# Performance work log

Measured on AMD Instinct MI355X. Metric: run time of the kernel, lower is better.

## Reference

```python
import jax, jax.numpy as jnp
import numpy as np

C_S = 128
C_T = 128
C_OUT = 128


def _proj(x, W, b):
    # 1x1x1 Conv3d == per-voxel linear over channel dim. x: [B, Cin, T, H, W]
    return jnp.einsum('oc,bcthw->bothw', W, x) + b[None, :, None, None, None]


def setup_inputs() -> dict:
    key = jax.random.key(0)
    ks = jax.random.split(key, 12)
    B, T, H, W = 4, 4, 32, 32
    spatial_features = jax.random.normal(ks[0], (B, T, C_S, H, W), dtype=jnp.float32)
    temporal_features = jax.random.normal(ks[1], (B, C_T, T, H, W), dtype=jnp.float32)
    def w(k, o, i):
        return jax.random.normal(k, (o, i), dtype=jnp.float32) * (i ** -0.5)
    return {
        'spatial_features': spatial_features,
        'temporal_features': temporal_features,
        'Wq': w(ks[2], C_OUT, C_S), 'bq': jnp.zeros((C_OUT,), jnp.float32),
        'Wk': w(ks[3], C_OUT, C_T), 'bk': jnp.zeros((C_OUT,), jnp.float32),
        'Wv': w(ks[4], C_OUT, C_T), 'bv': jnp.zeros((C_OUT,), jnp.float32),
        'Wo': w(ks[5], C_OUT, C_OUT), 'bo': jnp.zeros((C_OUT,), jnp.float32),
    }


def reference(spatial_features, temporal_features, Wq, bq, Wk, bk, Wv, bv, Wo, bo):
    B, T, C_s, H, W = spatial_features.shape
    N = T * H * W
    scale = C_OUT ** -0.5
    # permute(0,2,1,3,4): [B, T, C_s, H, W] -> [B, C_s, T, H, W]
    x_s = jnp.transpose(spatial_features, (0, 2, 1, 3, 4))
    q = _proj(x_s, Wq, bq)                 # [B, C_out, T, H, W]
    k = _proj(temporal_features, Wk, bk)   # [B, C_out, T, H, W]
    v = _proj(temporal_features, Wv, bv)   # [B, C_out, T, H, W]
    Q = q.reshape(B, C_OUT, N).transpose(0, 2, 1)  # [B, N, C]
    K = k.reshape(B, C_OUT, N)                     # [B, C, N]
    V = v.reshape(B, C_OUT, N).transpose(0, 2, 1)  # [B, N, C]
    attn = jax.nn.softmax(jnp.einsum('bnc,bcm->bnm', Q, K) * scale, axis=2)  # [B, N, N]
    out = jnp.einsum('bnm,bmc->bnc', attn, V)      # [B, N, C]
    out = out.transpose(0, 2, 1).reshape(B, C_OUT, T, H, W)
    return _proj(out, Wo, bo)
```

## Files before the change

kernel.cpp:

```cpp
#include <hip/hip_runtime.h>
#include <cstddef>

#define NDIM 4096
#define SCALE_L2E 0.12751741843533886f
#define BIAS_L2E  11.541560327111707f

typedef _Float16 h8 __attribute__((ext_vector_type(8)));
typedef _Float16 h4 __attribute__((ext_vector_type(4)));
typedef _Float16 h2 __attribute__((ext_vector_type(2)));
typedef float    f4 __attribute__((ext_vector_type(4)));

__device__ __forceinline__ void gld_lds16(const void* g, void* l) {
    __builtin_amdgcn_global_load_lds(
        (const __attribute__((address_space(1))) void*)g,
        (__attribute__((address_space(3))) void*)l, 16, 0, 0);
}

__device__ __forceinline__ h8 cvt_w_frag(const float* wp) {
    const float4 u0 = *(const float4*)wp;
    const float4 u1 = *(const float4*)(wp + 4);
    h8 f;
    f[0]=(_Float16)u0.x; f[1]=(_Float16)u0.y; f[2]=(_Float16)u0.z; f[3]=(_Float16)u0.w;
    f[4]=(_Float16)u1.x; f[5]=(_Float16)u1.y; f[6]=(_Float16)u1.z; f[7]=(_Float16)u1.w;
    return f;
}

__global__ __launch_bounds__(256) void prep_w_kernel(
    const float* __restrict__ Wq, const float* __restrict__ Wk,
    const float* __restrict__ Wv, const float* __restrict__ Wo,
    _Float16* __restrict__ Whf)
{
    const int gid = blockIdx.x * 256 + threadIdx.x;
    const int mat = gid >> 11, rem = gid & 2047;
    const int ot = rem >> 8, ks = (rem >> 6) & 3, l = rem & 63;
    const float* src = mat == 0 ? Wq : mat == 1 ? Wk : mat == 2 ? Wv : Wo;
    const h8 f = cvt_w_frag(src + (size_t)(16 * ot + (l & 15)) * 128 + 32 * ks + 8 * (l >> 4));
    *(h8*)(Whf + (size_t)gid * 8) = f;
}

__global__ __launch_bounds__(256, 3) void proj_qkv_kernel(
    const float* __restrict__ spatial, const float* __restrict__ temporal,
    const _Float16* __restrict__ Whf,
    const float* __restrict__ bq, const float* __restrict__ bk,
    const float* __restrict__ bv,
    _Float16* __restrict__ Qh, _Float16* __restrict__ Kh, _Float16* __restrict__ Vt)
{
    __shared__ __align__(16) _Float16 Xl[32 * 136];
    const int tid = threadIdx.x;
    const int n0  = blockIdx.x * 32;
    const int b   = blockIdx.y;
    const int p   = blockIdx.z;
    const float* __restrict__ bias = (p == 0) ? bq : (p == 1) ? bk : bv;

    {
        const float* src; size_t rs;
        if (p == 0) { const int t = n0 >> 10, hw0 = n0 & 1023;
            src = spatial + (((size_t)(b * 4 + t) * 128) << 10) + hw0; rs = 1024; }
        else { src = temporal + ((size_t)(b * 128) << 12) + n0; rs = 4096; }
        #pragma unroll
        for (int i = 0; i < 2; ++i) {
            const int ii = tid + 256 * i;
            const int c2 = ii >> 3, j = ii & 7;
            const float4 v0 = *(const float4*)(src + (size_t)(2 * c2) * rs + 4 * j);
            const float4 v1 = *(const float4*)(src + (size_t)(2 * c2 + 1) * rs + 4 * j);
            const float a0[4] = {v0.x, v0.y, v0.z, v0.w};
            const float a1[4] = {v1.x, v1.y, v1.z, v1.w};
            #pragma unroll
            for (int u = 0; u < 4; ++u) {
                h2 pk; pk[0] = (_Float16)a0[u]; pk[1] = (_Float16)a1[u];
                *(h2*)&Xl[(4 * j + u) * 136 + 2 * c2] = pk;
            }
        }
    }
    __syncthreads();

    const int w = tid >> 6, lane = tid & 63, n16 = tid & 15, q4 = (tid >> 4) & 3;

    h8 wf[2][4];
    #pragma unroll
    for (int otl = 0; otl < 2; ++otl)
        #pragma unroll
        for (int ks = 0; ks < 4; ++ks)
            wf[otl][ks] = *(const h8*)(Whf + ((size_t)(((p * 8 + 2 * w + otl) * 4 + ks)) << 9)
                                           + lane * 8);
    h8 xf[2][4];
    #pragma unroll
    for (int ns = 0; ns < 2; ++ns)
        #pragma unroll
        for (int ks = 0; ks < 4; ++ks)
            xf[ns][ks] = *(const h8*)&Xl[(16 * ns + n16) * 136 + 32 * ks + 8 * q4];

    if (p < 2) {
        f4 acc[2][2];
        #pragma unroll
        for (int i = 0; i < 2; ++i) { acc[i][0] = (f4)0.0f; acc[i][1] = (f4)0.0f; }
        #pragma unroll
        for (int otl = 0; otl < 2; ++otl)
            #pragma unroll
            for (int ns = 0; ns < 2; ++ns)
                #pragma unroll
                for (int ks = 0; ks < 4; ++ks)
                    acc[otl][ns] = __builtin_amdgcn_mfma_f32_16x16x32_f16(
                        wf[otl][ks], xf[ns][ks], acc[otl][ns], 0, 0, 0);
        _Float16* __restrict__ dst = (p == 0) ? Qh : Kh;
        #pragma unroll
        for (int otl = 0; otl < 2; ++otl) {
            const float4 bb = *(const float4*)&bias[16 * (2 * w + otl) + 4 * q4];
            #pragma unroll
            for (int ns = 0; ns < 2; ++ns) {
                h4 r;
                r[0]=(_Float16)(acc[otl][ns][0]+bb.x); r[1]=(_Float16)(acc[otl][ns][1]+bb.y);
                r[2]=(_Float16)(acc[otl][ns][2]+bb.z); r[3]=(_Float16)(acc[otl][ns][3]+bb.w);
                *(h4*)(dst + ((size_t)b * NDIM + n0 + 16 * ns + n16) * 128
                           + 16 * (2 * w + otl) + 4 * q4) = r;
            }
        }
    } else {
        f4 acc[2][2];
        #pragma unroll
        for (int i = 0; i < 2; ++i) { acc[i][0] = (f4)0.0f; acc[i][1] = (f4)0.0f; }
        #pragma unroll
        for (int ns = 0; ns < 2; ++ns)
            #pragma unroll
            for (int otl = 0; otl < 2; ++otl)
                #pragma unroll
                for (int ks = 0; ks < 4; ++ks)
                    acc[ns][otl] = __builtin_amdgcn_mfma_f32_16x16x32_f16(
                        xf[ns][ks], wf[otl][ks], acc[ns][otl], 0, 0, 0);
        #pragma unroll
        for (int ns = 0; ns < 2; ++ns)
            #pragma unroll
            for (int otl = 0; otl < 2; ++otl) {
                const float bb = bias[16 * (2 * w + otl) + n16];
                h4 r;
                r[0]=(_Float16)(acc[ns][otl][0]+bb); r[1]=(_Float16)(acc[ns][otl][1]+bb);
                r[2]=(_Float16)(acc[ns][otl][2]+bb); r[3]=(_Float16)(acc[ns][otl][3]+bb);
                *(h4*)(Vt + ((size_t)(b * 128 + 16 * (2 * w + otl) + n16) << 12)
                          + n0 + 16 * ns + 4 * q4) = r;
            }
    }
}

__global__ __launch_bounds__(256, 2) void attn_kernel(
    const _Float16* __restrict__ Qh, const _Float16* __restrict__ Kh,
    const _Float16* __restrict__ Vt, _Float16* __restrict__ Opart,
    float* __restrict__ lpart)
{
    __shared__ __align__(16) _Float16 sh[30720];

    const int tid  = threadIdx.x;
    const int w    = tid >> 6, lane = tid & 63;
    const int g    = w >> 1,  p    = w & 1;
    const int n16  = lane & 15, q4 = lane >> 4;

    const int id = blockIdx.x + 32 * blockIdx.y + 128 * blockIdx.z;
    const int pi = (id & 7) + 8 * (id >> 8);
    const int qt = (id >> 3) & 31;
    const int hf = pi & 3, b = pi >> 2;
    const int n0 = qt * 128;
    const int mb = hf * 1024;

    const int r4 = lane >> 4, c16 = lane & 15;
    const _Float16* kg0 = Kh + ((size_t)b * NDIM + mb + 8 * w + r4) * 128
                             + ((c16 * 8) ^ ((r4 & 7) << 3));
    const _Float16* kg1 = Kh + ((size_t)b * NDIM + mb + 8 * w + 4 + r4) * 128
                             + ((c16 * 8) ^ (((4 + r4) & 7) << 3));
    const int vr = lane >> 2, vc4 = lane & 3;
    const _Float16* vg0 = Vt + (((size_t)(b * 128 + 32 * w + vr)) << 12) + mb + vc4 * 8;
    const _Float16* vg1 = vg0 + ((size_t)16 << 12);

    const int kd = (8 * w) * 128;
    const int vd = (32 * w) * 32;

    gld_lds16(kg0, sh + kd);            gld_lds16(kg1, sh + kd + 512);
    gld_lds16(vg0, sh + 8192 + vd);     gld_lds16(vg1, sh + 8192 + vd + 512);
    kg0 += 32 * 128; kg1 += 32 * 128; vg0 += 32; vg1 += 32;

    h8 qf[4][4];
    {
        const _Float16* Qb = Qh + ((size_t)b * NDIM + n0 + 64 * g + n16) * 128;
        #pragma unroll
        for (int qs = 0; qs < 4; ++qs)
            #pragma unroll
            for (int ks = 0; ks < 4; ++ks)
                qf[qs][ks] = *(const h8*)(Qb + (size_t)(16 * qs) * 128 + 32 * ks + 8 * q4);
    }

    f4 oacc[4][4];
    #pragma unroll
    for (int i = 0; i < 4; ++i)
        #pragma unroll
        for (int j = 0; j < 4; ++j) oacc[i][j] = (f4)0.0f;
    float lsum[4] = {0.0f, 0.0f, 0.0f, 0.0f};

    const int kx = (n16 & 7) << 3;
    const int krow = (16 * p + n16) * 128;

    for (int it = 0; it < 32; ++it) {
        __syncthreads();
        const int cur = it & 1;
        _Float16* __restrict__ Pg = sh + 20480 + cur * 5120 + g * 2560;
        const _Float16* __restrict__ Pp = sh + 20480 + (cur ^ 1) * 5120 + g * 2560;

        if (it < 31) {
            _Float16* kdst = sh + (cur ^ 1) * 4096 + kd;
            gld_lds16(kg0, kdst); gld_lds16(kg1, kdst + 512);
            const int vst = (it + 1) % 3;
            _Float16* vdst = sh + 8192 + vst * 4096 + vd;
            gld_lds16(vg0, vdst); gld_lds16(vg1, vdst + 512);
            kg0 += 32 * 128; kg1 += 32 * 128; vg0 += 32; vg1 += 32;
        }

        if (it > 0) {
            const int vrd = (it - 1) % 3;
            const _Float16* __restrict__ VP = sh + 8192 + vrd * 4096;
            h8 pf[4], vf[4];
            #pragma unroll
            for (int qs = 0; qs < 4; ++qs)
                pf[qs] = *(const h8*)&Pp[(16 * qs + n16) * 40 + 8 * q4];
            #pragma unroll
            for (int ct = 0; ct < 4; ++ct)
                vf[ct] = *(const h8*)&VP[(64 * p + 16 * ct + n16) * 32 + 8 * q4];
            __builtin_amdgcn_s_setprio(1);
            #pragma unroll
            for (int qs = 0; qs < 4; ++qs)
                #pragma unroll
                for (int ct = 0; ct < 4; ++ct)
                    oacc[qs][ct] = __builtin_amdgcn_mfma_f32_16x16x32_f16(
                        pf[qs], vf[ct], oacc[qs][ct], 0, 0, 0);
            __builtin_amdgcn_s_setprio(0);
        }

        f4 sacc[4];
        #pragma unroll
        for (int qs = 0; qs < 4; ++qs) sacc[qs] = (f4)0.0f;
        {
            const _Float16* __restrict__ KB = sh + cur * 4096;
            h8 kf[4];
            #pragma unroll
            for (int ks = 0; ks < 4; ++ks)
                kf[ks] = *(const h8*)&KB[krow + ((32 * ks + 8 * q4) ^ kx)];
            __builtin_amdgcn_s_setprio(1);
            #pragma unroll
            for (int ks = 0; ks < 4; ++ks)
                #pragma unroll
                for (int qs = 0; qs < 4; ++qs)
                    sacc[qs] = __builtin_amdgcn_mfma_f32_16x16x32_f16(
                        kf[ks], qf[qs][ks], sacc[qs], 0, 0, 0);
            __builtin_amdgcn_s_setprio(0);
        }

        #pragma unroll
        for (int qs = 0; qs < 4; ++qs) {
            h4 pk;
            #pragma unroll
            for (int r = 0; r < 4; ++r) {
                const float e = __builtin_amdgcn_exp2f(fmaf(sacc[qs][r], SCALE_L2E, -BIAS_L2E));
                lsum[qs] += e;
                pk[r] = (_Float16)e;
            }
            *(h4*)&Pg[(16 * qs + n16) * 40 + 16 * p + 4 * q4] = pk;
        }
    }

    __syncthreads();
    {
        const _Float16* __restrict__ Pp = sh + 20480 + 5120 + g * 2560;
        const _Float16* __restrict__ VP = sh + 8192 + 1 * 4096;
        h8 pf[4], vf[4];
        #pragma unroll
        for (int qs = 0; qs < 4; ++qs)
            pf[qs] = *(const h8*)&Pp[(16 * qs + n16) * 40 + 8 * q4];
        #pragma unroll
        for (int ct = 0; ct < 4; ++ct)
            vf[ct] = *(const h8*)&VP[(64 * p + 16 * ct + n16) * 32 + 8 * q4];
        #pragma unroll
        for (int qs = 0; qs < 4; ++qs)
            #pragma unroll
            for (int ct = 0; ct < 4; ++ct)
                oacc[qs][ct] = __builtin_amdgcn_mfma_f32_16x16x32_f16(
                    pf[qs], vf[ct], oacc[qs][ct], 0, 0, 0);
    }

    #pragma unroll
    for (int qs = 0; qs < 4; ++qs) {
        lsum[qs] += __shfl_xor(lsum[qs], 16, 64);
        lsum[qs] += __shfl_xor(lsum[qs], 32, 64);
    }
    if (q4 == 0) {
        float* lb = lpart + ((size_t)((hf * 2 + p) * 4 + b)) * NDIM + n0 + 64 * g;
        #pragma unroll
        for (int qs = 0; qs < 4; ++qs) lb[16 * qs + n16] = lsum[qs];
    }

    __syncthreads();
    #pragma unroll
    for (int qs = 0; qs < 4; ++qs)
        #pragma unroll
        for (int ct = 0; ct < 4; ++ct)
            #pragma unroll
            for (int r = 0; r < 4; ++r)
                sh[(64 * g + 16 * qs + 4 * q4 + r) * 136 + 64 * p + 16 * ct + n16] =
                    (_Float16)oacc[qs][ct][r];
    __syncthreads();
    const size_t ob = ((size_t)(hf * 4 + b) * NDIM + n0) * 128;
    #pragma unroll
    for (int i = 0; i < 8; ++i) {
        const int ii  = tid + 256 * i;
        const int row = ii >> 4, c8 = (ii & 15) * 8;
        *(int4*)(Opart + ob + (size_t)row * 128 + c8) = *(const int4*)&sh[row * 136 + c8];
    }
}

__global__ __launch_bounds__(256, 2) void proj_final_kernel(
    const _Float16* __restrict__ Opart, const float* __restrict__ lpart,
    const _Float16* __restrict__ Whf, const float* __restrict__ bo,
    float* __restrict__ out)
{
    __shared__ __align__(16) _Float16 Xl[32 * 136];
    __shared__ float lrow[32];
    __shared__ __align__(16) float Ofin[128 * 36];
    const int tid = threadIdx.x;
    const int n0  = blockIdx.x * 32;
    const int b   = blockIdx.y;

    if (tid < 32) {
        float l = 0.0f;
        #pragma unroll
        for (int h8i = 0; h8i < 8; ++h8i)
            l += lpart[((size_t)(h8i * 4 + b)) * NDIM + n0 + tid];
        lrow[tid] = 1.0f / l;
    }
    float vals[2][8];
    int rows[2], c8s[2];
    #pragma unroll
    for (int i = 0; i < 2; ++i) {
        const int ii = tid + 256 * i;
        rows[i] = ii >> 4; c8s[i] = (ii & 15) * 8;
        #pragma unroll
        for (int j = 0; j < 8; ++j) vals[i][j] = 0.0f;
        #pragma unroll
        for (int hf = 0; hf < 4; ++hf) {
            const h8 o = *(const h8*)(Opart + ((size_t)(hf * 4 + b) * NDIM + n0 + rows[i]) * 128
                                      + c8s[i]);
            #pragma unroll
            for (int j = 0; j < 8; ++j) vals[i][j] += (float)o[j];
        }
    }
    __syncthreads();
    #pragma unroll
    for (int i = 0; i < 2; ++i) {
        const float linv = lrow[rows[i]];
        h8 r;
        #pragma unroll
        for (int j = 0; j < 8; ++j) r[j] = (_Float16)(vals[i][j] * linv);
        *(h8*)&Xl[rows[i] * 136 + c8s[i]] = r;
    }
    __syncthreads();

    const int w = tid >> 6, lane = tid & 63, n16 = tid & 15, q4 = (tid >> 4) & 3;

    h8 wf[2][4];
    #pragma unroll
    for (int otl = 0; otl < 2; ++otl)
        #pragma unroll
        for (int ks = 0; ks < 4; ++ks)
            wf[otl][ks] = *(const h8*)(Whf + ((size_t)(((3 * 8 + 2 * w + otl) * 4 + ks)) << 9)
                                           + lane * 8);
    h8 xf[2][4];
    #pragma unroll
    for (int ns = 0; ns < 2; ++ns)
        #pragma unroll
        for (int ks = 0; ks < 4; ++ks)
            xf[ns][ks] = *(const h8*)&Xl[(16 * ns + n16) * 136 + 32 * ks + 8 * q4];

    f4 acc[2][2];
    #pragma unroll
    for (int i = 0; i < 2; ++i) { acc[i][0] = (f4)0.0f; acc[i][1] = (f4)0.0f; }
    #pragma unroll
    for (int otl = 0; otl < 2; ++otl)
        #pragma unroll
        for (int ns = 0; ns < 2; ++ns)
            #pragma unroll
            for (int ks = 0; ks < 4; ++ks)
                acc[otl][ns] = __builtin_amdgcn_mfma_f32_16x16x32_f16(
                    wf[otl][ks], xf[ns][ks], acc[otl][ns], 0, 0, 0);

    #pragma unroll
    for (int otl = 0; otl < 2; ++otl) {
        const float4 bb = *(const float4*)&bo[16 * (2 * w + otl) + 4 * q4];
        const float bias[4] = {bb.x, bb.y, bb.z, bb.w};
        #pragma unroll
        for (int ns = 0; ns < 2; ++ns)
            #pragma unroll
            for (int r = 0; r < 4; ++r)
                Ofin[(16 * (2 * w + otl) + 4 * q4 + r) * 36 + 16 * ns + n16] =
                    acc[otl][ns][r] + bias[r];
    }
    __syncthreads();
    #pragma unroll
    for (int i = 0; i < 4; ++i) {
        const int ii  = tid + 256 * i;
        const int row = ii >> 3, j = ii & 7;
        *(float4*)(out + (((size_t)(b * 128 + row)) << 12) + n0 + 4 * j) =
            *(const float4*)&Ofin[row * 36 + 4 * j];
    }
}

extern "C" void kernel_launch(void* const* d_in, const int* in_sizes, int n_in,
                              void* d_out, int out_size, void* d_ws, size_t ws_size,
                              hipStream_t stream)
{
    const float* spatial  = (const float*)d_in[0];
    const float* temporal = (const float*)d_in[1];
    const float* Wq = (const float*)d_in[2];
    const float* bq = (const float*)d_in[3];
    const float* Wk = (const float*)d_in[4];
    const float* bk = (const float*)d_in[5];
    const float* Wv = (const float*)d_in[6];
    const float* bv = (const float*)d_in[7];
    const float* Wo = (const float*)d_in[8];
    const float* bo = (const float*)d_in[9];

    char* ws = (char*)d_ws;
    _Float16* Qh    = (_Float16*)(ws);
    _Float16* Kh    = (_Float16*)(ws + (4u  << 20));
    _Float16* Vt    = (_Float16*)(ws + (8u  << 20));
    _Float16* Opart = (_Float16*)(ws + (12u << 20));
    float*    lpart = (float*)   (ws + (28u << 20));
    _Float16* Whf   = (_Float16*)(ws + (28u << 20) + (512u << 10));

    prep_w_kernel<<<32, 256, 0, stream>>>(Wq, Wk, Wv, Wo, Whf);
    proj_qkv_kernel<<<dim3(128, 4, 3), 256, 0, stream>>>(
        spatial, temporal, Whf, bq, bk, bv, Qh, Kh, Vt);
    attn_kernel<<<dim3(32, 4, 4), 256, 0, stream>>>(Qh, Kh, Vt, Opart, lpart);
    proj_final_kernel<<<dim3(128, 4), 256, 0, stream>>>(Opart, lpart, Whf, bo,
                                                        (float*)d_out);
}
```

Measured before the change: 136.4 us.

## Switch attention to 32x32x16 MFMA with register-resident P and per-wave query rows

Rewrites the attention inner loop to use 32x32x16 MFMA tiles, where each wave owns 32 query rows and the full key tile. The exponentiated scores stay in registers as the A operand of the PV MFMA, so the LDS staging buffer for P and its extra synchronisation are removed. The change also swaps the V triple buffer for a double buffer with XOR swizzling and halves the lpart partial sums per row. It cuts LDS traffic and shared memory size, but adds more accumulator registers, which may pressure occupancy.

```diff
diff --git a/kernel.cpp b/kernel.cpp
--- a/kernel.cpp
+++ b/kernel.cpp
@@ -9,6 +9,7 @@
 typedef _Float16 h4 __attribute__((ext_vector_type(4)));
 typedef _Float16 h2 __attribute__((ext_vector_type(2)));
 typedef float    f4 __attribute__((ext_vector_type(4)));
+typedef float    f32x16 __attribute__((ext_vector_type(16)));
 
 __device__ __forceinline__ void gld_lds16(const void* g, void* l) {
     __builtin_amdgcn_global_load_lds(
@@ -146,12 +147,12 @@
     const _Float16* __restrict__ Vt, _Float16* __restrict__ Opart,
     float* __restrict__ lpart)
 {
-    __shared__ __align__(16) _Float16 sh[30720];
+    __shared__ __align__(16) _Float16 sh[17408];
 
     const int tid  = threadIdx.x;
     const int w    = tid >> 6, lane = tid & 63;
-    const int g    = w >> 1,  p    = w & 1;
-    const int n16  = lane & 15, q4 = lane >> 4;
+    const int g    = w;
+    const int lq   = lane & 31, kh = lane >> 5;
 
     const int id = blockIdx.x + 32 * blockIdx.y + 128 * blockIdx.z;
     const int pi = (id & 7) + 8 * (id >> 8);
@@ -162,13 +163,13 @@
 
     const int r4 = lane >> 4, c16 = lane & 15;
     const _Float16* kg0 = Kh + ((size_t)b * NDIM + mb + 8 * w + r4) * 128
-                             + ((c16 * 8) ^ ((r4 & 7) << 3));
+                             + ((c16 * 8) ^ (r4 << 3));
     const _Float16* kg1 = Kh + ((size_t)b * NDIM + mb + 8 * w + 4 + r4) * 128
-                             + ((c16 * 8) ^ (((4 + r4) & 7) << 3));
+                             + ((c16 * 8) ^ ((4 + r4) << 3));
     const int vr = lane >> 2, vc4 = lane & 3;
-    const _Float16* vg0 = Vt + (((size_t)(b * 128 + 32 * w + vr)) << 12) + mb + vc4 * 8;
+    const _Float16* vg0 = Vt + (((size_t)(b * 128 + 32 * w + vr)) << 12) + mb
+                             + 8 * (vc4 ^ ((vr >> 1) & 3));
     const _Float16* vg1 = vg0 + ((size_t)16 << 12);
-
     const int kd = (8 * w) * 128;
     const int vd = (32 * w) * 32;
 
@@ -176,132 +177,117 @@
     gld_lds16(vg0, sh + 8192 + vd);     gld_lds16(vg1, sh + 8192 + vd + 512);
     kg0 += 32 * 128; kg1 += 32 * 128; vg0 += 32; vg1 += 32;
 
-    h8 qf[4][4];
+    h8 qf[8];
     {
-        const _Float16* Qb = Qh + ((size_t)b * NDIM + n0 + 64 * g + n16) * 128;
-        #pragma unroll
-        for (int qs = 0; qs < 4; ++qs)
-            #pragma unroll
-            for (int ks = 0; ks < 4; ++ks)
-                qf[qs][ks] = *(const h8*)(Qb + (size_t)(16 * qs) * 128 + 32 * ks + 8 * q4);
-    }
-
-    f4 oacc[4][4];
-    #pragma unroll
-    for (int i = 0; i < 4; ++i)
-        #pragma unroll
-        for (int j = 0; j < 4; ++j) oacc[i][j] = (f4)0.0f;
-    float lsum[4] = {0.0f, 0.0f, 0.0f, 0.0f};
-
-    const int kx = (n16 & 7) << 3;
-    const int krow = (16 * p + n16) * 128;
+        const _Float16* Qb = Qh + ((size_t)b * NDIM + n0 + 32 * g + lq) * 128 + 8 * kh;
+        #pragma unroll
+        for (int ks = 0; ks < 8; ++ks)
+            qf[ks] = *(const h8*)(Qb + 16 * ks);
+    }
+
+    f32x16 oacc[4];
+    #pragma unroll
+    for (int i = 0; i < 4; ++i) oacc[i] = (f32x16)0.0f;
+    float la0 = 0.0f, la1 = 0.0f;
+    h8 pf0, pf1, vfr[4][2];
+
+    const int krow = lq * 128;
+    const int kxr  = lq & 7;
 
     for (int it = 0; it < 32; ++it) {
         __syncthreads();
         const int cur = it & 1;
-        _Float16* __restrict__ Pg = sh + 20480 + cur * 5120 + g * 2560;
-        const _Float16* __restrict__ Pp = sh + 20480 + (cur ^ 1) * 5120 + g * 2560;
 
         if (it < 31) {
             _Float16* kdst = sh + (cur ^ 1) * 4096 + kd;
+            _Float16* vdst = sh + 8192 + (cur ^ 1) * 4096 + vd;
             gld_lds16(kg0, kdst); gld_lds16(kg1, kdst + 512);
-            const int vst = (it + 1) % 3;
-            _Float16* vdst = sh + 8192 + vst * 4096 + vd;
             gld_lds16(vg0, vdst); gld_lds16(vg1, vdst + 512);
             kg0 += 32 * 128; kg1 += 32 * 128; vg0 += 32; vg1 += 32;
         }
 
-        if (it > 0) {
-            const int vrd = (it - 1) % 3;
-            const _Float16* __restrict__ VP = sh + 8192 + vrd * 4096;
-            h8 pf[4], vf[4];
-            #pragma unroll
-            for (int qs = 0; qs < 4; ++qs)
-                pf[qs] = *(const h8*)&Pp[(16 * qs + n16) * 40 + 8 * q4];
-            #pragma unroll
-            for (int ct = 0; ct < 4; ++ct)
-                vf[ct] = *(const h8*)&VP[(64 * p + 16 * ct + n16) * 32 + 8 * q4];
-            __builtin_amdgcn_s_setprio(1);
-            #pragma unroll
-            for (int qs = 0; qs < 4; ++qs)
-                #pragma unroll
-                for (int ct = 0; ct < 4; ++ct)
-                    oacc[qs][ct] = __builtin_amdgcn_mfma_f32_16x16x32_f16(
-                        pf[qs], vf[ct], oacc[qs][ct], 0, 0, 0);
-            __builtin_amdgcn_s_setprio(0);
-        }
-
-        f4 sacc[4];
-        #pragma unroll
-        for (int qs = 0; qs < 4; ++qs) sacc[qs] = (f4)0.0f;
+        f32x16 sa = (f32x16)0.0f, sb = (f32x16)0.0f;
         {
             const _Float16* __restrict__ KB = sh + cur * 4096;
-            h8 kf[4];
-            #pragma unroll
-            for (int ks = 0; ks < 4; ++ks)
-                kf[ks] = *(const h8*)&KB[krow + ((32 * ks + 8 * q4) ^ kx)];
+            #pragma unroll
+            for (int ks = 0; ks < 4; ++ks) {
+                const h8 kf = *(const h8*)&KB[krow + 8 * ((2 * ks + kh) ^ kxr)];
+                sa = __builtin_amdgcn_mfma_f32_32x32x16_f16(kf, qf[ks], sa, 0, 0, 0);
+            }
+            #pragma unroll
+            for (int ks = 4; ks < 8; ++ks) {
+                const h8 kf = *(const h8*)&KB[krow + 8 * ((2 * ks + kh) ^ kxr)];
+                sb = __builtin_amdgcn_mfma_f32_32x32x16_f16(kf, qf[ks], sb, 0, 0, 0);
+            }
+        }
+
+        if (it > 0) {
             __builtin_amdgcn_s_setprio(1);
             #pragma unroll
-            for (int ks = 0; ks < 4; ++ks)
+            for (int cb = 0; cb < 4; ++cb) {
+                oacc[cb] = __builtin_amdgcn_mfma_f32_32x32x16_f16(pf0, vfr[cb][0], oacc[cb], 0, 0, 0);
+                oacc[cb] = __builtin_amdgcn_mfma_f32_32x32x16_f16(pf1, vfr[cb][1], oacc[cb], 0, 0, 0);
+            }
+            __builtin_amdgcn_s_setprio(0);
+        }
+
+        {
+            const _Float16* __restrict__ VB = sh + 8192 + cur * 4096;
+            #pragma unroll
+            for (int cb = 0; cb < 4; ++cb) {
+                const int cbase = (32 * cb + lq) * 32;
+                const int sx = lq & 6;
                 #pragma unroll
-                for (int qs = 0; qs < 4; ++qs)
-                    sacc[qs] = __builtin_amdgcn_mfma_f32_16x16x32_f16(
-                        kf[ks], qf[qs][ks], sacc[qs], 0, 0, 0);
-            __builtin_amdgcn_s_setprio(0);
-        }
-
-        #pragma unroll
-        for (int qs = 0; qs < 4; ++qs) {
-            h4 pk;
-            #pragma unroll
-            for (int r = 0; r < 4; ++r) {
-                const float e = __builtin_amdgcn_exp2f(fmaf(sacc[qs][r], SCALE_L2E, -BIAS_L2E));
-                lsum[qs] += e;
-                pk[r] = (_Float16)e;
-            }
-            *(h4*)&Pg[(16 * qs + n16) * 40 + 16 * p + 4 * q4] = pk;
-        }
-    }
-
-    __syncthreads();
+                for (int kk = 0; kk < 2; ++kk) {
+                    const h4 lo = *(const h4*)&VB[cbase + 4 * ((4 * kk + kh) ^ sx)];
+                    const h4 hi = *(const h4*)&VB[cbase + 4 * ((4 * kk + 2 + kh) ^ sx)];
+                    h8 v;
+                    v[0]=lo[0]; v[1]=lo[1]; v[2]=lo[2]; v[3]=lo[3];
+                    v[4]=hi[0]; v[5]=hi[1]; v[6]=hi[2]; v[7]=hi[3];
+                    vfr[cb][kk] = v;
+                }
+            }
+        }
+
+        #pragma unroll
+        for (int r = 0; r < 8; ++r) {
+            const float e = __builtin_amdgcn_exp2f(
+                fmaf(sa[r], SCALE_L2E, fmaf(sb[r], SCALE_L2E, -BIAS_L2E)));
+            if (r & 1) la1 += e; else la0 += e;
+            pf0[r] = (_Float16)e;
+        }
+        #pragma unroll
+        for (int r = 8; r < 16; ++r) {
+            const float e = __builtin_amdgcn_exp2f(
+                fmaf(sa[r], SCALE_L2E, fmaf(sb[r], SCALE_L2E, -BIAS_L2E)));
+            if (r & 1) la1 += e; else la0 += e;
+            pf1[r - 8] = (_Float16)e;
+        }
+    }
+
     {
-        const _Float16* __restrict__ Pp = sh + 20480 + 5120 + g * 2560;
-        const _Float16* __restrict__ VP = sh + 8192 + 1 * 4096;
-        h8 pf[4], vf[4];
-        #pragma unroll
-        for (int qs = 0; qs < 4; ++qs)
-            pf[qs] = *(const h8*)&Pp[(16 * qs + n16) * 40 + 8 * q4];
-        #pragma unroll
-        for (int ct = 0; ct < 4; ++ct)
-            vf[ct] = *(const h8*)&VP[(64 * p + 16 * ct + n16) * 32 + 8 * q4];
-        #pragma unroll
-        for (int qs = 0; qs < 4; ++qs)
-            #pragma unroll
-            for (int ct = 0; ct < 4; ++ct)
-                oacc[qs][ct] = __builtin_amdgcn_mfma_f32_16x16x32_f16(
-                    pf[qs], vf[ct], oacc[qs][ct], 0, 0, 0);
-    }
-
-    #pragma unroll
-    for (int qs = 0; qs < 4; ++qs) {
-        lsum[qs] += __shfl_xor(lsum[qs], 16, 64);
-        lsum[qs] += __shfl_xor(lsum[qs], 32, 64);
-    }
-    if (q4 == 0) {
-        float* lb = lpart + ((size_t)((hf * 2 + p) * 4 + b)) * NDIM + n0 + 64 * g;
-        #pragma unroll
-        for (int qs = 0; qs < 4; ++qs) lb[16 * qs + n16] = lsum[qs];
-    }
-
-    __syncthreads();
-    #pragma unroll
-    for (int qs = 0; qs < 4; ++qs)
-        #pragma unroll
-        for (int ct = 0; ct < 4; ++ct)
-            #pragma unroll
-            for (int r = 0; r < 4; ++r)
-                sh[(64 * g + 16 * qs + 4 * q4 + r) * 136 + 64 * p + 16 * ct + n16] =
-                    (_Float16)oacc[qs][ct][r];
+        __builtin_amdgcn_s_setprio(1);
+        #pragma unroll
+        for (int cb = 0; cb < 4; ++cb) {
+            oacc[cb] = __builtin_amdgcn_mfma_f32_32x32x16_f16(pf0, vfr[cb][0], oacc[cb], 0, 0, 0);
+            oacc[cb] = __builtin_amdgcn_mfma_f32_32x32x16_f16(pf1, vfr[cb][1], oacc[cb], 0, 0, 0);
+        }
+        __builtin_amdgcn_s_setprio(0);
+    }
+
+    float lsum = la0 + la1;
+    lsum += __shfl_xor(lsum, 32, 64);
+    if (lane < 32)
+        lpart[((size_t)(hf * 4 + b)) * NDIM + n0 + 32 * g + lq] = lsum;
+
+    __syncthreads();
+    #pragma unroll
+    for (int cb = 0; cb < 4; ++cb)
+        #pragma unroll
+        for (int r = 0; r < 16; ++r) {
+            const int qrow = 32 * g + (r & 3) + 8 * (r >> 2) + 4 * kh;
+            sh[qrow * 136 + 32 * cb + lq] = (_Float16)oacc[cb][r];
+        }
     __syncthreads();
     const size_t ob = ((size_t)(hf * 4 + b) * NDIM + n0) * 128;
     #pragma unroll
@@ -327,8 +313,8 @@
     if (tid < 32) {
         float l = 0.0f;
         #pragma unroll
-        for (int h8i = 0; h8i < 8; ++h8i)
-            l += lpart[((size_t)(h8i * 4 + b)) * NDIM + n0 + tid];
+        for (int h4i = 0; h4i < 4; ++h4i)
+            l += lpart[((size_t)(h4i * 4 + b)) * NDIM + n0 + tid];
         lrow[tid] = 1.0f / l;
     }
     float vals[2][8];
```

New measurement: 144.5 us. 1.06x slower.

## Double attention block to 512 threads with 32-row query slices per wave group

Applied to the files above, without the earlier changes.

The attention kernel now runs 8 waves per block instead of 4. Each wave group handles 32 query rows rather than 64, which halves the per-thread Q fragments and accumulators and so lowers register pressure. Each thread issues one K and one V global-to-LDS load per tile instead of two. The V tile in LDS gets an XOR swizzle to cut bank conflicts. More waves share each K/V tile, which should improve latency hiding, at the cost of more synchronisation participants per barrier.

```diff
diff --git a/kernel.cpp b/kernel.cpp
--- a/kernel.cpp
+++ b/kernel.cpp
@@ -141,7 +141,7 @@
     }
 }
 
-__global__ __launch_bounds__(256, 2) void attn_kernel(
+__global__ __launch_bounds__(512, 4) void attn_kernel(
     const _Float16* __restrict__ Qh, const _Float16* __restrict__ Kh,
     const _Float16* __restrict__ Vt, _Float16* __restrict__ Opart,
     float* __restrict__ lpart)
@@ -160,70 +160,64 @@
     const int n0 = qt * 128;
     const int mb = hf * 1024;
 
-    const int r4 = lane >> 4, c16 = lane & 15;
-    const _Float16* kg0 = Kh + ((size_t)b * NDIM + mb + 8 * w + r4) * 128
-                             + ((c16 * 8) ^ ((r4 & 7) << 3));
-    const _Float16* kg1 = Kh + ((size_t)b * NDIM + mb + 8 * w + 4 + r4) * 128
-                             + ((c16 * 8) ^ (((4 + r4) & 7) << 3));
-    const int vr = lane >> 2, vc4 = lane & 3;
-    const _Float16* vg0 = Vt + (((size_t)(b * 128 + 32 * w + vr)) << 12) + mb + vc4 * 8;
-    const _Float16* vg1 = vg0 + ((size_t)16 << 12);
-
-    const int kd = (8 * w) * 128;
-    const int vd = (32 * w) * 32;
-
-    gld_lds16(kg0, sh + kd);            gld_lds16(kg1, sh + kd + 512);
-    gld_lds16(vg0, sh + 8192 + vd);     gld_lds16(vg1, sh + 8192 + vd + 512);
-    kg0 += 32 * 128; kg1 += 32 * 128; vg0 += 32; vg1 += 32;
-
-    h8 qf[4][4];
+    const int kr = tid >> 4, kc = tid & 15;
+    const _Float16* kg = Kh + ((size_t)b * NDIM + mb + kr) * 128
+                            + 8 * (kc ^ (kr & 7));
+    const int vr = tid >> 2, vc = tid & 3;
+    const _Float16* vg = Vt + (((size_t)(b * 128 + vr)) << 12) + mb
+                            + 8 * (vc ^ ((vr >> 1) & 3));
+    const int ld = tid * 8;
+
+    gld_lds16(kg, sh + ld);
+    gld_lds16(vg, sh + 8192 + ld);
+    kg += 32 * 128; vg += 32;
+
+    h8 qf[2][4];
     {
-        const _Float16* Qb = Qh + ((size_t)b * NDIM + n0 + 64 * g + n16) * 128;
-        #pragma unroll
-        for (int qs = 0; qs < 4; ++qs)
+        const _Float16* Qb = Qh + ((size_t)b * NDIM + n0 + 32 * g + n16) * 128;
+        #pragma unroll
+        for (int qs = 0; qs < 2; ++qs)
             #pragma unroll
             for (int ks = 0; ks < 4; ++ks)
                 qf[qs][ks] = *(const h8*)(Qb + (size_t)(16 * qs) * 128 + 32 * ks + 8 * q4);
     }
 
-    f4 oacc[4][4];
-    #pragma unroll
-    for (int i = 0; i < 4; ++i)
+    f4 oacc[2][4];
+    #pragma unroll
+    for (int i = 0; i < 2; ++i)
         #pragma unroll
         for (int j = 0; j < 4; ++j) oacc[i][j] = (f4)0.0f;
-    float lsum[4] = {0.0f, 0.0f, 0.0f, 0.0f};
-
-    const int kx = (n16 & 7) << 3;
+    float lsum[2] = {0.0f, 0.0f};
+
+    const int kx   = (n16 & 7) << 3;
     const int krow = (16 * p + n16) * 128;
 
     for (int it = 0; it < 32; ++it) {
         __syncthreads();
         const int cur = it & 1;
-        _Float16* __restrict__ Pg = sh + 20480 + cur * 5120 + g * 2560;
-        const _Float16* __restrict__ Pp = sh + 20480 + (cur ^ 1) * 5120 + g * 2560;
+        _Float16* __restrict__ Pb = sh + 20480 + cur * 5120;
+        const _Float16* __restrict__ Pp = sh + 20480 + (cur ^ 1) * 5120;
 
         if (it < 31) {
-            _Float16* kdst = sh + (cur ^ 1) * 4096 + kd;
-            gld_lds16(kg0, kdst); gld_lds16(kg1, kdst + 512);
-            const int vst = (it + 1) % 3;
-            _Float16* vdst = sh + 8192 + vst * 4096 + vd;
-            gld_lds16(vg0, vdst); gld_lds16(vg1, vdst + 512);
-            kg0 += 32 * 128; kg1 += 32 * 128; vg0 += 32; vg1 += 32;
+            gld_lds16(kg, sh + (cur ^ 1) * 4096 + ld);
+            gld_lds16(vg, sh + 8192 + ((it + 1) % 3) * 4096 + ld);
+            kg += 32 * 128; vg += 32;
         }
 
         if (it > 0) {
-            const int vrd = (it - 1) % 3;
-            const _Float16* __restrict__ VP = sh + 8192 + vrd * 4096;
-            h8 pf[4], vf[4];
-            #pragma unroll
-            for (int qs = 0; qs < 4; ++qs)
-                pf[qs] = *(const h8*)&Pp[(16 * qs + n16) * 40 + 8 * q4];
-            #pragma unroll
-            for (int ct = 0; ct < 4; ++ct)
-                vf[ct] = *(const h8*)&VP[(64 * p + 16 * ct + n16) * 32 + 8 * q4];
+            const _Float16* __restrict__ VP = sh + 8192 + ((it - 1) % 3) * 4096;
+            h8 pf[2], vf[4];
+            #pragma unroll
+            for (int qs = 0; qs < 2; ++qs)
+                pf[qs] = *(const h8*)&Pp[(32 * g + 16 * qs + n16) * 40 + 8 * q4];
+            #pragma unroll
+            for (int ct = 0; ct < 4; ++ct) {
+                const int r = 64 * p + 16 * ct + n16;
+                vf[ct] = *(const h8*)&VP[r * 32 + 8 * (q4 ^ ((r >> 1) & 3))];
+            }
             __builtin_amdgcn_s_setprio(1);
             #pragma unroll
-            for (int qs = 0; qs < 4; ++qs)
+            for (int qs = 0; qs < 2; ++qs)
                 #pragma unroll
                 for (int ct = 0; ct < 4; ++ct)
                     oacc[qs][ct] = __builtin_amdgcn_mfma_f32_16x16x32_f16(
@@ -231,9 +225,8 @@
             __builtin_amdgcn_s_setprio(0);
         }
 
-        f4 sacc[4];
-        #pragma unroll
-        for (int qs = 0; qs < 4; ++qs) sacc[qs] = (f4)0.0f;
+        f4 sacc[2];
+        sacc[0] = (f4)0.0f; sacc[1] = (f4)0.0f;
         {
             const _Float16* __restrict__ KB = sh + cur * 4096;
             h8 kf[4];
@@ -244,14 +237,14 @@
             #pragma unroll
             for (int ks = 0; ks < 4; ++ks)
                 #pragma unroll
-                for (int qs = 0; qs < 4; ++qs)
+                for (int qs = 0; qs < 2; ++qs)
                     sacc[qs] = __builtin_amdgcn_mfma_f32_16x16x32_f16(
                         kf[ks], qf[qs][ks], sacc[qs], 0, 0, 0);
             __builtin_amdgcn_s_setprio(0);
         }
 
         #pragma unroll
-        for (int qs = 0; qs < 4; ++qs) {
+        for (int qs = 0; qs < 2; ++qs) {
             h4 pk;
             #pragma unroll
             for (int r = 0; r < 4; ++r) {
@@ -259,23 +252,25 @@
                 lsum[qs] += e;
                 pk[r] = (_Float16)e;
             }
-            *(h4*)&Pg[(16 * qs + n16) * 40 + 16 * p + 4 * q4] = pk;
+            *(h4*)&Pb[(32 * g + 16 * qs + n16) * 40 + 16 * p + 4 * q4] = pk;
         }
     }
 
     __syncthreads();
     {
-        const _Float16* __restrict__ Pp = sh + 20480 + 5120 + g * 2560;
+        const _Float16* __restrict__ Pp = sh + 20480 + 5120;
         const _Float16* __restrict__ VP = sh + 8192 + 1 * 4096;
-        h8 pf[4], vf[4];
-        #pragma unroll
-        for (int qs = 0; qs < 4; ++qs)
-            pf[qs] = *(const h8*)&Pp[(16 * qs + n16) * 40 + 8 * q4];
-        #pragma unroll
-        for (int ct = 0; ct < 4; ++ct)
-            vf[ct] = *(const h8*)&VP[(64 * p + 16 * ct + n16) * 32 + 8 * q4];
-        #pragma unroll
-        for (int qs = 0; qs < 4; ++qs)
+        h8 pf[2], vf[4];
+        #pragma unroll
+        for (int qs = 0; qs < 2; ++qs)
+            pf[qs] = *(const h8*)&Pp[(32 * g + 16 * qs + n16) * 40 + 8 * q4];
+        #pragma unroll
+        for (int ct = 0; ct < 4; ++ct) {
+            const int r = 64 * p + 16 * ct + n16;
+            vf[ct] = *(const h8*)&VP[r * 32 + 8 * (q4 ^ ((r >> 1) & 3))];
+        }
+        #pragma unroll
+        for (int qs = 0; qs < 2; ++qs)
             #pragma unroll
             for (int ct = 0; ct < 4; ++ct)
                 oacc[qs][ct] = __builtin_amdgcn_mfma_f32_16x16x32_f16(
@@ -283,30 +278,30 @@
     }
 
     #pragma unroll
-    for (int qs = 0; qs < 4; ++qs) {
+    for (int qs = 0; qs < 2; ++qs) {
         lsum[qs] += __shfl_xor(lsum[qs], 16, 64);
         lsum[qs] += __shfl_xor(lsum[qs], 32, 64);
     }
     if (q4 == 0) {
-        float* lb = lpart + ((size_t)((hf * 2 + p) * 4 + b)) * NDIM + n0 + 64 * g;
-        #pragma unroll
-        for (int qs = 0; qs < 4; ++qs) lb[16 * qs + n16] = lsum[qs];
-    }
-
-    __syncthreads();
-    #pragma unroll
-    for (int qs = 0; qs < 4; ++qs)
+        float* lb = lpart + ((size_t)((hf * 2 + p) * 4 + b)) * NDIM + n0 + 32 * g;
+        #pragma unroll
+        for (int qs = 0; qs < 2; ++qs) lb[16 * qs + n16] = lsum[qs];
+    }
+
+    __syncthreads();
+    #pragma unroll
+    for (int qs = 0; qs < 2; ++qs)
         #pragma unroll
         for (int ct = 0; ct < 4; ++ct)
             #pragma unroll
             for (int r = 0; r < 4; ++r)
-                sh[(64 * g + 16 * qs + 4 * q4 + r) * 136 + 64 * p + 16 * ct + n16] =
+                sh[(32 * g + 16 * qs + 4 * q4 + r) * 136 + 64 * p + 16 * ct + n16] =
                     (_Float16)oacc[qs][ct][r];
     __syncthreads();
     const size_t ob = ((size_t)(hf * 4 + b) * NDIM + n0) * 128;
     #pragma unroll
-    for (int i = 0; i < 8; ++i) {
-        const int ii  = tid + 256 * i;
+    for (int i = 0; i < 4; ++i) {
+        const int ii  = tid + 512 * i;
         const int row = ii >> 4, c8 = (ii & 15) * 8;
         *(int4*)(Opart + ob + (size_t)row * 128 + c8) = *(const int4*)&sh[row * 136 + c8];
     }
@@ -433,7 +428,7 @@
     prep_w_kernel<<<32, 256, 0, stream>>>(Wq, Wk, Wv, Wo, Whf);
     proj_qkv_kernel<<<dim3(128, 4, 3), 256, 0, stream>>>(
         spatial, temporal, Whf, bq, bk, bv, Qh, Kh, Vt);
-    attn_kernel<<<dim3(32, 4, 4), 256, 0, stream>>>(Qh, Kh, Vt, Opart, lpart);
+    attn_kernel<<<dim3(32, 4, 4), 512, 0, stream>>>(Qh, Kh, Vt, Opart, lpart);
     proj_final_kernel<<<dim3(128, 4), 256, 0, stream>>>(Opart, lpart, Whf, bo,
                                                         (float*)d_out);
 }
```

After: 139.4 us. 1.02x slower.
